# Performance work log

Hardware: AMD Instinct MI355X
Metric: run time of the kernel (lower is better)

The kernel has to match this reference:

```python
import jax, jax.numpy as jnp
import numpy as np
import math

L = 6; D = 768; NH = 12; DH = D // NH; V = 2048; CTX = 512; B = 16; T = 512
PAD_ID = 0; PAD_X = 18; PAD_Y = 32; N_ACTIONS = 9


def _layernorm(x, s, b, eps=1e-5):
    m = jnp.mean(x, axis=-1, keepdims=True)
    v = jnp.mean((x - m) ** 2, axis=-1, keepdims=True)
    return (x - m) * jax.lax.rsqrt(v + eps) * s + b


def setup_inputs() -> dict:
    key = jax.random.key(0)
    ks = jax.random.split(key, 16)
    s = 0.02
    x_emb = jax.random.normal(ks[4], (19, D), jnp.float32) * s
    x_emb = x_emb.at[PAD_X].set(0.0)  # padding_idx row is zero in torch
    y_emb = jax.random.normal(ks[5], (33, D), jnp.float32) * s
    y_emb = y_emb.at[PAD_Y].set(0.0)
    return {
        "history_cards": jax.random.randint(ks[0], (B, T), 0, V),
        "history_players": jax.random.randint(ks[1], (B, T), 0, 2),
        "deck": jax.random.randint(ks[2], (B, 8), 0, V),
        "opp_deck": jax.random.randint(ks[3], (B, 8), 0, V),
        "tok_emb": jax.random.normal(ks[6], (V, D), jnp.float32) * s,
        "player_emb": jax.random.normal(ks[7], (2, D), jnp.float32) * s,
        "pos_emb": jax.random.normal(ks[8], (CTX, D), jnp.float32) * s,
        "x_emb": x_emb,
        "y_emb": y_emb,
        "ln1_s": jnp.ones((L, D), jnp.float32),
        "ln1_b": jnp.zeros((L, D), jnp.float32),
        "qkv_w": jax.random.normal(ks[9], (L, D, 3 * D), jnp.float32) * s,
        "qkv_b": jnp.zeros((L, 3 * D), jnp.float32),
        "proj_w": jax.random.normal(ks[10], (L, D, D), jnp.float32) * s,
        "proj_b": jnp.zeros((L, D), jnp.float32),
        "ln2_s": jnp.ones((L, D), jnp.float32),
        "ln2_b": jnp.zeros((L, D), jnp.float32),
        "fc1_w": jax.random.normal(ks[11], (L, D, 4 * D), jnp.float32) * s,
        "fc1_b": jnp.zeros((L, 4 * D), jnp.float32),
        "fc2_w": jax.random.normal(ks[12], (L, 4 * D, D), jnp.float32) * s,
        "fc2_b": jnp.zeros((L, D), jnp.float32),
        "lnf_s": jnp.ones((D,), jnp.float32),
        "lnf_b": jnp.zeros((D,), jnp.float32),
        "head_w": jax.random.normal(ks[13], (D, N_ACTIONS), jnp.float32) * s,
        "head_b": jnp.zeros((N_ACTIONS,), jnp.float32),
    }


def reference(history_cards, history_players, deck, opp_deck,
              tok_emb, player_emb, pos_emb, x_emb, y_emb,
              ln1_s, ln1_b, qkv_w, qkv_b, proj_w, proj_b,
              ln2_s, ln2_b, fc1_w, fc1_b, fc2_w, fc2_b,
              lnf_s, lnf_b, head_w, head_b):
    Bc, Tc = history_cards.shape
    attn_mask = history_cards != PAD_ID                      # (B,T) True = valid
    all_pad = ~jnp.any(attn_mask, axis=1)
    attn_mask = attn_mask.at[:, 0].set(attn_mask[:, 0] | all_pad)

    # multi-embedding sum (history_x/history_y are None => padding rows = 0)
    h = (tok_emb[history_cards]
         + player_emb[jnp.clip(history_players, 0, 1)]
         + x_emb[PAD_X] + y_emb[PAD_Y]
         + jnp.mean(tok_emb[deck], axis=1, keepdims=True)
         + jnp.mean(tok_emb[opp_deck], axis=1, keepdims=True))
    x = h + pos_emb[:Tc][None]                               # (B,T,D)

    causal = jnp.tril(jnp.ones((Tc, Tc), bool))
    mask = causal[None, None, :, :] & attn_mask[:, None, None, :]  # (B,1,T,T)
    neg_inf = jnp.float32(-jnp.inf)
    scale = 1.0 / math.sqrt(DH)

    for i in range(L):
        # attention
        xn = _layernorm(x, ln1_s[i], ln1_b[i])
        qkv = xn @ qkv_w[i] + qkv_b[i]
        q, k, v = jnp.split(qkv, 3, axis=-1)
        q = q.reshape(Bc, Tc, NH, DH)
        k = k.reshape(Bc, Tc, NH, DH)
        v = v.reshape(Bc, Tc, NH, DH)
        scores = jnp.einsum('bihd,bjhd->bhij', q, k) * scale
        scores = jnp.where(mask, scores, neg_inf)
        w = jax.nn.softmax(scores, axis=-1)
        w = jnp.nan_to_num(w, nan=0.0, posinf=0.0, neginf=0.0)
        y = jnp.einsum('bhij,bjhd->bihd', w, v).reshape(Bc, Tc, D)
        x = x + (y @ proj_w[i] + proj_b[i])
        # MLP
        xn = _layernorm(x, ln2_s[i], ln2_b[i])
        hmid = jax.nn.gelu(xn @ fc1_w[i] + fc1_b[i], approximate=False)
        x = x + (hmid @ fc2_w[i] + fc2_b[i])

    x = _layernorm(x, lnf_s, lnf_b)
    last_idx = jnp.clip(jnp.sum(attn_mask.astype(jnp.int32), axis=1) - 1, 0, None)
    last_h = x[jnp.arange(Bc), last_idx]                     # (B,D)
    return last_h @ head_w + head_b                          # (B,9)
```

## Files before the change

kernel.cpp:

```cpp
#include <hip/hip_runtime.h>
#include <hip/hip_bf16.h>
#include <math.h>

typedef __hip_bfloat16 bf16;
typedef __bf16 bf16x8 __attribute__((ext_vector_type(8)));
typedef float f32x4 __attribute__((ext_vector_type(4)));

__device__ __forceinline__ float b2f(bf16 v){ return __bfloat162float(v); }
__device__ __forceinline__ bf16  f2b(float v){ return __float2bfloat16(v); }

__device__ __forceinline__ float gelu_f(float v){
    float y = v * (1.f + 0.044715f * v * v);
    return v / (1.f + __expf(-1.5957691216057308f * y));
}

__device__ __forceinline__ void gl_lds16(const bf16* g, bf16* l) {
    __builtin_amdgcn_global_load_lds((const __attribute__((address_space(1))) unsigned int*)g,
                                     (__attribute__((address_space(3))) unsigned int*)l, 16, 0, 0);
}

__device__ __forceinline__ uint2 pack4bf(const float* v){
    union { unsigned short e[4]; uint2 u; } pk;
    #pragma unroll
    for (int r = 0; r < 4; r++) pk.e[r] = __builtin_bit_cast(unsigned short, f2b(v[r]));
    return pk.u;
}

__global__ __launch_bounds__(256) void deckmean_k(const int* __restrict__ deck, const int* __restrict__ opp,
                                                  const float* __restrict__ tok, float* __restrict__ deckm)
{
    int b = blockIdx.x, w = blockIdx.y;
    const int* dk = (w ? opp : deck) + b * 8;
    int idx[8];
    #pragma unroll
    for (int j = 0; j < 8; j++) idx[j] = dk[j];
    float* out = deckm + (size_t)(w * 16 + b) * 768;
    for (int d = threadIdx.x; d < 768; d += 256) {
        float s = 0.f;
        #pragma unroll
        for (int j = 0; j < 8; j++) s += tok[(size_t)idx[j] * 768 + d];
        out[d] = s * 0.125f;
    }
}

__global__ __launch_bounds__(512) void mask_k(const int* __restrict__ cards, int* __restrict__ maskb,
                                              int* __restrict__ lastidx)
{
    int b = blockIdx.x, t = threadIdx.x;
    int m = (cards[b * 512 + t] != 0) ? 1 : 0;
    maskb[b * 512 + t] = m;
    __shared__ int red[512];
    red[t] = m; __syncthreads();
    for (int st = 256; st > 0; st >>= 1) { if (t < st) red[t] += red[t + st]; __syncthreads(); }
    if (t == 0) {
        int cnt = red[0];
        if (cnt == 0) { maskb[b * 512] = 1; cnt = 1; }
        lastidx[b] = cnt - 1;
    }
}

__global__ __launch_bounds__(256) void embed_k(const int* __restrict__ cards, const int* __restrict__ players,
                                               const float* __restrict__ tok, const float* __restrict__ pemb,
                                               const float* __restrict__ pos, const float* __restrict__ deckm,
                                               float* __restrict__ x)
{
    int t = blockIdx.x;
    int b = t >> 9, ti = t & 511;
    int cd = cards[t];
    int p = players[t]; p = p < 0 ? 0 : (p > 1 ? 1 : p);
    const float* tr  = tok  + (size_t)cd * 768;
    const float* pr  = pemb + (size_t)p  * 768;
    const float* po  = pos  + (size_t)ti * 768;
    const float* dm = deckm + (size_t)b * 768;
    const float* om = deckm + (size_t)(16 + b) * 768;
    float* xr = x + (size_t)t * 768;
    for (int d = threadIdx.x; d < 768; d += 256)
        xr[d] = tr[d] + pr[d] + po[d] + dm[d] + om[d];
}

__global__ __launch_bounds__(192) void ln_k(const float* __restrict__ x, const float* __restrict__ s,
                                            const float* __restrict__ b, bf16* __restrict__ out)
{
    int row = blockIdx.x, tid = threadIdx.x;
    float4 v = ((const float4*)(x + (size_t)row * 768))[tid];
    float sum = v.x + v.y + v.z + v.w;
    float sq  = v.x * v.x + v.y * v.y + v.z * v.z + v.w * v.w;
    #pragma unroll
    for (int off = 32; off > 0; off >>= 1) {
        sum += __shfl_xor(sum, off, 64);
        sq  += __shfl_xor(sq,  off, 64);
    }
    __shared__ float red[6];
    int wv = tid >> 6;
    if ((tid & 63) == 0) { red[wv] = sum; red[3 + wv] = sq; }
    __syncthreads();
    float S = red[0] + red[1] + red[2];
    float Q = red[3] + red[4] + red[5];
    float mean = S * (1.f / 768.f);
    float var  = Q * (1.f / 768.f) - mean * mean;
    float rstd = rsqrtf(var + 1e-5f);
    float4 sv = ((const float4*)s)[tid];
    float4 bv = ((const float4*)b)[tid];
    float o[4] = { (v.x - mean) * rstd * sv.x + bv.x, (v.y - mean) * rstd * sv.y + bv.y,
                   (v.z - mean) * rstd * sv.z + bv.z, (v.w - mean) * rstd * sv.w + bv.w };
    ((uint2*)(out + (size_t)row * 768))[tid] = pack4bf(o);
}

__global__ __launch_bounds__(256) void transpose4_k(const float* __restrict__ qw, const float* __restrict__ pw,
                                                    const float* __restrict__ f1, const float* __restrict__ f2,
                                                    bf16* __restrict__ oq, bf16* __restrict__ op,
                                                    bf16* __restrict__ o1, bf16* __restrict__ o2)
{
    int t = blockIdx.x;
    const float* in; bf16* out; int K, N, nbx;
    if (t < 432)       { in = qw; out = oq; K = 768;  N = 2304; nbx = 36; }
    else if (t < 576)  { in = pw; out = op; K = 768;  N = 768;  t -= 432;  nbx = 12; }
    else if (t < 1152) { in = f1; out = o1; K = 768;  N = 3072; t -= 576;  nbx = 48; }
    else               { in = f2; out = o2; K = 3072; N = 768;  t -= 1152; nbx = 12; }
    int n0 = (t % nbx) * 64, k0 = (t / nbx) * 64;
    int kq = threadIdx.x & 15, nq = threadIdx.x >> 4;
    float4 rr[4];
    #pragma unroll
    for (int r = 0; r < 4; r++)
        rr[r] = *(const float4*)&in[(size_t)(k0 + kq * 4 + r) * N + n0 + nq * 4];
    const float* fp = (const float*)rr;
    #pragma unroll
    for (int c = 0; c < 4; c++) {
        float v[4] = { fp[c], fp[4 + c], fp[8 + c], fp[12 + c] };
        *(uint2*)&out[(size_t)(n0 + nq * 4 + c) * K + k0 + kq * 4] = pack4bf(v);
    }
}

__global__ __launch_bounds__(256) void gemm128_k(const bf16* __restrict__ A, const bf16* __restrict__ BT,
                                                 const float* __restrict__ bias,
                                                 float* __restrict__ outF, bf16* __restrict__ outB,
                                                 int N, int K, int act, int nb)
{
    __shared__ __align__(16) bf16 Al[128 * 64];
    __shared__ __align__(16) bf16 Bl[128 * 64];
    const int tid = threadIdx.x;
    const int lane = tid & 63, wave = tid >> 6;
    const int quad = lane >> 4, l16 = lane & 15;
    const int wm = wave >> 1, wn = wave & 1;

    const int bid = blockIdx.x;
    const int xcd = bid & 7, slot = bid >> 3;
    const int m_loc = slot / nb, nbl = slot - m_loc * nb;
    const int m0 = (xcd * 8 + m_loc) * 128, n0 = nbl * 128;

    f32x4 acc[4][4] = {};
    const int srow = wave * 32;
    const int grow = srow + (lane >> 3);
    const int gcol = (lane & 7) * 8;

    for (int k0 = 0; k0 < K; k0 += 64) {
        #pragma unroll
        for (int i = 0; i < 4; i++) {
            gl_lds16(&A [(size_t)(m0 + grow + i * 8) * K + k0 + gcol], &Al[(srow + i * 8) * 64]);
            gl_lds16(&BT[(size_t)(n0 + grow + i * 8) * K + k0 + gcol], &Bl[(srow + i * 8) * 64]);
        }
        __syncthreads();
        #pragma unroll
        for (int kk = 0; kk < 64; kk += 32) {
            bf16x8 af[4], bfr[4];
            #pragma unroll
            for (int t = 0; t < 4; t++) {
                af[t]  = __builtin_bit_cast(bf16x8, *(const uint4*)(&Al[(wm * 64 + t * 16 + l16) * 64 + kk + quad * 8]));
                bfr[t] = __builtin_bit_cast(bf16x8, *(const uint4*)(&Bl[(wn * 64 + t * 16 + l16) * 64 + kk + quad * 8]));
            }
            #pragma unroll
            for (int tm = 0; tm < 4; tm++)
                #pragma unroll
                for (int tn = 0; tn < 4; tn++)
                    acc[tm][tn] = __builtin_amdgcn_mfma_f32_16x16x32_bf16(bfr[tn], af[tm], acc[tm][tn], 0, 0, 0);
        }
        __syncthreads();
    }

    float4 bv[4];
    #pragma unroll
    for (int tn = 0; tn < 4; tn++)
        bv[tn] = *(const float4*)&bias[n0 + wn * 64 + tn * 16 + quad * 4];

    #pragma unroll
    for (int tm = 0; tm < 4; tm++) {
        int m = m0 + wm * 64 + tm * 16 + l16;
        #pragma unroll
        for (int tn = 0; tn < 4; tn++) {
            int nbase = n0 + wn * 64 + tn * 16 + quad * 4;
            float v[4] = { acc[tm][tn][0] + bv[tn].x, acc[tm][tn][1] + bv[tn].y,
                           acc[tm][tn][2] + bv[tn].z, acc[tm][tn][3] + bv[tn].w };
            if (act) {
                #pragma unroll
                for (int r = 0; r < 4; r++) v[r] = gelu_f(v[r]);
            }
            size_t off = (size_t)m * N + nbase;
            if (outB) *(uint2*)&outB[off] = pack4bf(v);
            else      *(float4*)&outF[off] = make_float4(v[0], v[1], v[2], v[3]);
        }
    }
}

__global__ __launch_bounds__(256) void gemm64_k(const bf16* __restrict__ A, const bf16* __restrict__ BT,
                                                const float* __restrict__ bias,
                                                float* __restrict__ x, int N, int K, int nb)
{
    __shared__ __align__(16) bf16 Al[64 * 64];
    __shared__ __align__(16) bf16 Bl[128 * 64];
    const int tid = threadIdx.x;
    const int lane = tid & 63, wave = tid >> 6;
    const int quad = lane >> 4, l16 = lane & 15;
    const int wm = wave >> 1, wn = wave & 1;

    const int bid = blockIdx.x;
    const int xcd = bid & 7, slot = bid >> 3;
    const int m_loc = slot / nb, nbl = slot - m_loc * nb;
    const int m0 = (xcd * 16 + m_loc) * 64, n0 = nbl * 128;

    f32x4 acc[2][4] = {};
    const int srow = wave * 8 + (lane >> 3);
    const int gcol = (lane & 7) * 8;

    for (int k0 = 0; k0 < K; k0 += 64) {
        #pragma unroll
        for (int i = 0; i < 2; i++)
            gl_lds16(&A [(size_t)(m0 + srow + i * 32) * K + k0 + gcol], &Al[(wave * 8 + i * 32) * 64]);
        #pragma unroll
        for (int i = 0; i < 4; i++)
            gl_lds16(&BT[(size_t)(n0 + srow + i * 32) * K + k0 + gcol], &Bl[(wave * 8 + i * 32) * 64]);
        __syncthreads();
        #pragma unroll
        for (int kk = 0; kk < 64; kk += 32) {
            bf16x8 af[2], bfr[4];
            #pragma unroll
            for (int t = 0; t < 2; t++)
                af[t]  = __builtin_bit_cast(bf16x8, *(const uint4*)(&Al[(wm * 32 + t * 16 + l16) * 64 + kk + quad * 8]));
            #pragma unroll
            for (int t = 0; t < 4; t++)
                bfr[t] = __builtin_bit_cast(bf16x8, *(const uint4*)(&Bl[(wn * 64 + t * 16 + l16) * 64 + kk + quad * 8]));
            #pragma unroll
            for (int tm = 0; tm < 2; tm++)
                #pragma unroll
                for (int tn = 0; tn < 4; tn++)
                    acc[tm][tn] = __builtin_amdgcn_mfma_f32_16x16x32_bf16(bfr[tn], af[tm], acc[tm][tn], 0, 0, 0);
        }
        __syncthreads();
    }

    float4 bv[4];
    #pragma unroll
    for (int tn = 0; tn < 4; tn++)
        bv[tn] = *(const float4*)&bias[n0 + wn * 64 + tn * 16 + quad * 4];

    #pragma unroll
    for (int tm = 0; tm < 2; tm++) {
        int m = m0 + wm * 32 + tm * 16 + l16;
        #pragma unroll
        for (int tn = 0; tn < 4; tn++) {
            int nbase = n0 + wn * 64 + tn * 16 + quad * 4;
            float* xp = &x[(size_t)m * N + nbase];
            float4 xo = *(float4*)xp;
            xo.x += acc[tm][tn][0] + bv[tn].x;
            xo.y += acc[tm][tn][1] + bv[tn].y;
            xo.z += acc[tm][tn][2] + bv[tn].z;
            xo.w += acc[tm][tn][3] + bv[tn].w;
            *(float4*)xp = xo;
        }
    }
}

__global__ __launch_bounds__(256) void attn_k(const bf16* __restrict__ qkv, const int* __restrict__ mask,
                                              bf16* __restrict__ y)
{
    const int qt = blockIdx.x, h = blockIdx.y, b = blockIdx.z;
    const int qbase = qt * 128, tokb = b * 512;
    __shared__ __align__(16) unsigned short Kl[128][72];
    __shared__ __align__(16) unsigned short Vt[64][136];
    __shared__ __align__(16) unsigned short Ptq[4][16][136];
    __shared__ float mkf[128];

    const int tid = threadIdx.x, wave = tid >> 6, lane = tid & 63;
    const int quad = lane >> 4, l16 = lane & 15;

    bf16x8 bq[2][2];
    #pragma unroll
    for (int qc = 0; qc < 2; qc++) {
        const bf16* qp = &qkv[(size_t)(tokb + qbase + wave * 32 + qc * 16 + l16) * 2304 + h * 64];
        bq[qc][0] = __builtin_bit_cast(bf16x8, *(const uint4*)(qp + quad * 8));
        bq[qc][1] = __builtin_bit_cast(bf16x8, *(const uint4*)(qp + 32 + quad * 8));
    }

    float m_i[2] = { -INFINITY, -INFINITY }, l_i[2] = { 0.f, 0.f };
    f32x4 Oacc[2][4] = {};

    const int nst = qt + 1;
    for (int s = 0; s < nst; s++) {
        const int j0 = s * 128;
        __syncthreads();
        {
            int key = tid >> 1, c0 = (tid & 1) * 32;
            const bf16* kg = &qkv[(size_t)(tokb + j0 + key) * 2304 + 768  + h * 64 + c0];
            const bf16* vg = &qkv[(size_t)(tokb + j0 + key) * 2304 + 1536 + h * 64 + c0];
            #pragma unroll
            for (int q = 0; q < 4; q++)
                *(uint4*)&Kl[key][c0 + q * 8] = *(const uint4*)(kg + q * 8);
            union { uint4 u[4]; unsigned short e[32]; } vv;
            #pragma unroll
            for (int q = 0; q < 4; q++) vv.u[q] = *(const uint4*)(vg + q * 8);
            #pragma unroll
            for (int j = 0; j < 32; j++) Vt[c0 + j][key] = vv.e[j];
            if (tid < 128) mkf[tid] = mask[b * 512 + j0 + tid] ? 0.f : -INFINITY;
        }
        __syncthreads();

        #pragma unroll
        for (int qc = 0; qc < 2; qc++) {
            const int qi = qbase + wave * 32 + qc * 16 + l16;

            f32x4 sc[8] = {};
            #pragma unroll
            for (int kcc = 0; kcc < 8; kcc++) {
                bf16x8 af0 = __builtin_bit_cast(bf16x8, *(const uint4*)&Kl[kcc * 16 + l16][quad * 8]);
                bf16x8 af1 = __builtin_bit_cast(bf16x8, *(const uint4*)&Kl[kcc * 16 + l16][32 + quad * 8]);
                sc[kcc] = __builtin_amdgcn_mfma_f32_16x16x32_bf16(af0, bq[qc][0], sc[kcc], 0, 0, 0);
                sc[kcc] = __builtin_amdgcn_mfma_f32_16x16x32_bf16(af1, bq[qc][1], sc[kcc], 0, 0, 0);
            }

            float pv[8][4];
            float mx = -INFINITY;
            #pragma unroll
            for (int kcc = 0; kcc < 8; kcc++) {
                float4 mk4 = *(const float4*)&mkf[kcc * 16 + quad * 4];
                float mkr[4] = { mk4.x, mk4.y, mk4.z, mk4.w };
                #pragma unroll
                for (int r = 0; r < 4; r++) {
                    int krel = kcc * 16 + quad * 4 + r;
                    float sval = (j0 + krel <= qi) ? (sc[kcc][r] * 0.125f + mkr[r]) : -INFINITY;
                    pv[kcc][r] = sval;
                    mx = fmaxf(mx, sval);
                }
            }
            mx = fmaxf(mx, __shfl_xor(mx, 16, 64));
            mx = fmaxf(mx, __shfl_xor(mx, 32, 64));
            float mn = fmaxf(m_i[qc], mx);
            float alpha = (mn == -INFINITY) ? 1.f : __expf(m_i[qc] - mn);
            float lsum = 0.f;
            #pragma unroll
            for (int kcc = 0; kcc < 8; kcc++)
                #pragma unroll
                for (int r = 0; r < 4; r++) {
                    float pp = (pv[kcc][r] == -INFINITY) ? 0.f : __expf(pv[kcc][r] - mn);
                    pv[kcc][r] = pp; lsum += pp;
                }
            lsum += __shfl_xor(lsum, 16, 64);
            lsum += __shfl_xor(lsum, 32, 64);
            m_i[qc] = mn; l_i[qc] = alpha * l_i[qc] + lsum;

            #pragma unroll
            for (int kcc = 0; kcc < 8; kcc++)
                *(uint2*)&Ptq[wave][l16][kcc * 16 + quad * 4] = pack4bf(pv[kcc]);
            #pragma unroll
            for (int mc = 0; mc < 4; mc++)
                #pragma unroll
                for (int r = 0; r < 4; r++) Oacc[qc][mc][r] *= alpha;

            __syncthreads();

            #pragma unroll
            for (int kcc = 0; kcc < 4; kcc++) {
                bf16x8 pb = __builtin_bit_cast(bf16x8, *(const uint4*)&Ptq[wave][l16][kcc * 32 + quad * 8]);
                #pragma unroll
                for (int mc = 0; mc < 4; mc++) {
                    bf16x8 vf = __builtin_bit_cast(bf16x8, *(const uint4*)&Vt[mc * 16 + l16][kcc * 32 + quad * 8]);
                    Oacc[qc][mc] = __builtin_amdgcn_mfma_f32_16x16x32_bf16(vf, pb, Oacc[qc][mc], 0, 0, 0);
                }
            }
        }
    }

    #pragma unroll
    for (int qc = 0; qc < 2; qc++) {
        float inv = (l_i[qc] > 0.f) ? 1.f / l_i[qc] : 0.f;
        const int tok = tokb + qbase + wave * 32 + qc * 16 + l16;
        #pragma unroll
        for (int mc = 0; mc < 4; mc++) {
            float v[4] = { Oacc[qc][mc][0] * inv, Oacc[qc][mc][1] * inv,
                           Oacc[qc][mc][2] * inv, Oacc[qc][mc][3] * inv };
            *(uint2*)&y[(size_t)tok * 768 + h * 64 + mc * 16 + quad * 4] = pack4bf(v);
        }
    }
}

__global__ __launch_bounds__(256) void head_k(const float* __restrict__ x, const int* __restrict__ lastidx,
                                              const float* __restrict__ ls, const float* __restrict__ lb,
                                              const float* __restrict__ hw, const float* __restrict__ hb,
                                              float* __restrict__ out)
{
    int b = blockIdx.x, tid = threadIdx.x;
    const float* xr = x + ((size_t)(b * 512 + lastidx[b])) * 768;
    float v0 = xr[tid], v1 = xr[tid + 256], v2 = xr[tid + 512];
    __shared__ float rs[256], rq[256];
    rs[tid] = v0 + v1 + v2; rq[tid] = v0 * v0 + v1 * v1 + v2 * v2;
    __syncthreads();
    for (int st = 128; st > 0; st >>= 1) {
        if (tid < st) { rs[tid] += rs[tid + st]; rq[tid] += rq[tid + st]; }
        __syncthreads();
    }
    float mean = rs[0] * (1.f / 768.f);
    float var  = rq[0] * (1.f / 768.f) - mean * mean;
    float rstd = rsqrtf(var + 1e-5f);
    float part[9];
    #pragma unroll
    for (int a = 0; a < 9; a++) part[a] = 0.f;
    float vv[3] = { v0, v1, v2 };
    #pragma unroll
    for (int e = 0; e < 3; e++) {
        int d = tid + e * 256;
        float xnv = (vv[e] - mean) * rstd * ls[d] + lb[d];
        #pragma unroll
        for (int a = 0; a < 9; a++) part[a] += xnv * hw[d * 9 + a];
    }
    __shared__ float r9[9][256];
    #pragma unroll
    for (int a = 0; a < 9; a++) r9[a][tid] = part[a];
    __syncthreads();
    for (int st = 128; st > 0; st >>= 1) {
        if (tid < st) {
            for (int a = 0; a < 9; a++) r9[a][tid] += r9[a][tid + st];
        }
        __syncthreads();
    }
    if (tid < 9) out[b * 9 + tid] = r9[tid][0] + hb[tid];
}

extern "C" void kernel_launch(void* const* d_in, const int* in_sizes, int n_in,
                              void* d_out, int out_size, void* d_ws, size_t ws_size,
                              hipStream_t stream) {
    const int*   cards   = (const int*)  d_in[0];
    const int*   players = (const int*)  d_in[1];
    const int*   deck    = (const int*)  d_in[2];
    const int*   oppd    = (const int*)  d_in[3];
    const float* tok     = (const float*)d_in[4];
    const float* pemb    = (const float*)d_in[5];
    const float* pos     = (const float*)d_in[6];
    const float* ln1s  = (const float*)d_in[9];
    const float* ln1b  = (const float*)d_in[10];
    const float* qkvw  = (const float*)d_in[11];
    const float* qkvb  = (const float*)d_in[12];
    const float* projw = (const float*)d_in[13];
    const float* projb = (const float*)d_in[14];
    const float* ln2s  = (const float*)d_in[15];
    const float* ln2b  = (const float*)d_in[16];
    const float* fc1w  = (const float*)d_in[17];
    const float* fc1b  = (const float*)d_in[18];
    const float* fc2w  = (const float*)d_in[19];
    const float* fc2b  = (const float*)d_in[20];
    const float* lnfs  = (const float*)d_in[21];
    const float* lnfb  = (const float*)d_in[22];
    const float* hw    = (const float*)d_in[23];
    const float* hb    = (const float*)d_in[24];
    float* out = (float*)d_out;

    char* p = (char*)d_ws;
    auto alloc = [&](size_t bytes) { char* q = p; p += (bytes + 255) & ~((size_t)255); return q; };
    float* x     = (float*)alloc(8192ull * 768 * 4);
    bf16*  xn    = (bf16*) alloc(8192ull * 768 * 2);
    bf16*  big   = (bf16*) alloc(8192ull * 3072 * 2);
    bf16*  wt    = (bf16*) alloc(7077888ull * 2);
    float* deckm = (float*)alloc(2ull * 16 * 768 * 4);
    int*   maskb = (int*)  alloc(8192ull * 4);
    int*   lasti = (int*)  alloc(64);

    bf16* wq = wt;
    bf16* wp = wq + 2304ull * 768;
    bf16* w1 = wp + 768ull * 768;
    bf16* w2 = w1 + 3072ull * 768;

    deckmean_k<<<dim3(16, 2), 256, 0, stream>>>(deck, oppd, tok, deckm);
    mask_k<<<16, 512, 0, stream>>>(cards, maskb, lasti);
    embed_k<<<8192, 256, 0, stream>>>(cards, players, tok, pemb, pos, deckm, x);

    for (int i = 0; i < 6; i++) {
        transpose4_k<<<1728, 256, 0, stream>>>(
            qkvw + (size_t)i * 768 * 2304, projw + (size_t)i * 768 * 768,
            fc1w + (size_t)i * 768 * 3072, fc2w + (size_t)i * 3072 * 768,
            wq, wp, w1, w2);

        ln_k<<<8192, 192, 0, stream>>>(x, ln1s + i * 768, ln1b + i * 768, xn);
        gemm128_k<<<64 * 18, 256, 0, stream>>>(xn, wq, qkvb + i * 2304, nullptr, big, 2304, 768, 0, 18);
        attn_k<<<dim3(4, 12, 16), 256, 0, stream>>>(big, maskb, xn);
        gemm64_k<<<128 * 6, 256, 0, stream>>>(xn, wp, projb + i * 768, x, 768, 768, 6);
        ln_k<<<8192, 192, 0, stream>>>(x, ln2s + i * 768, ln2b + i * 768, xn);
        gemm128_k<<<64 * 24, 256, 0, stream>>>(xn, w1, fc1b + i * 3072, nullptr, big, 3072, 768, 1, 24);
        gemm64_k<<<128 * 6, 256, 0, stream>>>(big, w2, fc2b + i * 768, x, 768, 3072, 6);
    }

    head_k<<<16, 256, 0, stream>>>(x, lasti, lnfs, lnfb, hw, hb, out);
}
```

Measured before the change: 2.050 ms.

## Replace 128x128 GEMM with double-buffered 256x256 swizzled-LDS MFMA kernel

Swaps the QKV and FC1 GEMM kernel for a 512-thread, 256x256-tile kernel. It double-buffers A and B tiles in LDS, prefetches the next K-tile while issuing MFMAs, and XOR-swizzles the LDS layout to avoid bank conflicts. It adds explicit barriers, waitcnt control and setprio around MFMA bursts, and remaps workgroups across XCDs. The aim is more data reuse per loaded tile and hiding global-load latency. The cost is 128KB of LDS per block, which limits occupancy, and a small grid (288 and 384 blocks) that may leave an unbalanced tail on the CUs.

```diff
diff --git a/kernel.cpp b/kernel.cpp
--- a/kernel.cpp
+++ b/kernel.cpp
@@ -24,6 +24,12 @@
     #pragma unroll
     for (int r = 0; r < 4; r++) pk.e[r] = __builtin_bit_cast(unsigned short, f2b(v[r]));
     return pk.u;
+}
+
+__device__ __forceinline__ void phase_bar() {
+    __builtin_amdgcn_sched_barrier(0);
+    __builtin_amdgcn_s_barrier();
+    __builtin_amdgcn_sched_barrier(0);
 }
 
 __global__ __launch_bounds__(256) void deckmean_k(const int* __restrict__ deck, const int* __restrict__ opp,
@@ -131,74 +137,122 @@
     }
 }
 
-__global__ __launch_bounds__(256) void gemm128_k(const bf16* __restrict__ A, const bf16* __restrict__ BT,
-                                                 const float* __restrict__ bias,
-                                                 float* __restrict__ outF, bf16* __restrict__ outB,
-                                                 int N, int K, int act, int nb)
-{
-    __shared__ __align__(16) bf16 Al[128 * 64];
-    __shared__ __align__(16) bf16 Bl[128 * 64];
-    const int tid = threadIdx.x;
-    const int lane = tid & 63, wave = tid >> 6;
+__global__ __launch_bounds__(512, 2) void gemm256_k(const bf16* __restrict__ A, const bf16* __restrict__ BT,
+                                                    const float* __restrict__ bias, bf16* __restrict__ out,
+                                                    int N, int K, int act, int nbn)
+{
+    __shared__ __align__(16) bf16 Asb[2][256 * 64];
+    __shared__ __align__(16) bf16 Bsb[2][256 * 64];
+
+    const int tid  = threadIdx.x;
+    const int lane = tid & 63, wid = tid >> 6;
     const int quad = lane >> 4, l16 = lane & 15;
-    const int wm = wave >> 1, wn = wave & 1;
-
-    const int bid = blockIdx.x;
-    const int xcd = bid & 7, slot = bid >> 3;
-    const int m_loc = slot / nb, nbl = slot - m_loc * nb;
-    const int m0 = (xcd * 8 + m_loc) * 128, n0 = nbl * 128;
-
-    f32x4 acc[4][4] = {};
-    const int srow = wave * 32;
-    const int grow = srow + (lane >> 3);
-    const int gcol = (lane & 7) * 8;
-
-    for (int k0 = 0; k0 < K; k0 += 64) {
-        #pragma unroll
-        for (int i = 0; i < 4; i++) {
-            gl_lds16(&A [(size_t)(m0 + grow + i * 8) * K + k0 + gcol], &Al[(srow + i * 8) * 64]);
-            gl_lds16(&BT[(size_t)(n0 + grow + i * 8) * K + k0 + gcol], &Bl[(srow + i * 8) * 64]);
-        }
-        __syncthreads();
-        #pragma unroll
-        for (int kk = 0; kk < 64; kk += 32) {
-            bf16x8 af[4], bfr[4];
-            #pragma unroll
-            for (int t = 0; t < 4; t++) {
-                af[t]  = __builtin_bit_cast(bf16x8, *(const uint4*)(&Al[(wm * 64 + t * 16 + l16) * 64 + kk + quad * 8]));
-                bfr[t] = __builtin_bit_cast(bf16x8, *(const uint4*)(&Bl[(wn * 64 + t * 16 + l16) * 64 + kk + quad * 8]));
-            }
-            #pragma unroll
-            for (int tm = 0; tm < 4; tm++)
-                #pragma unroll
-                for (int tn = 0; tn < 4; tn++)
-                    acc[tm][tn] = __builtin_amdgcn_mfma_f32_16x16x32_bf16(bfr[tn], af[tm], acc[tm][tn], 0, 0, 0);
-        }
-        __syncthreads();
+    const int wr = wid >> 2, wc = wid & 3;
+    const int xr  = l16 & 7;
+    const int cg0 = quad ^ xr;
+    const int cg1 = cg0 ^ 4;
+
+    const int nwg  = gridDim.x;
+    const int wgid = ((int)blockIdx.x & 7) * (nwg >> 3) + ((int)blockIdx.x >> 3);
+    const int mt = wgid / nbn, nt = wgid - mt * nbn;
+    const int m0 = mt * 256, n0 = nt * 256;
+
+    const int srow = wid * 8 + (lane >> 3);
+    const int scg  = (lane & 7) ^ (lane >> 3);
+    const bf16* sa[4]; const bf16* sb[4];
+    #pragma unroll
+    for (int s = 0; s < 4; s++) {
+        sa[s] = A  + (size_t)(m0 + s * 64 + srow) * K + scg * 8;
+        sb[s] = BT + (size_t)(n0 + s * 64 + srow) * K + scg * 8;
+    }
+
+#define STG_A(s, b) gl_lds16(sa[s], &Asb[b][((s) * 64 + wid * 8) * 64])
+#define STG_B(s, b) gl_lds16(sb[s], &Bsb[b][((s) * 64 + wid * 8) * 64])
+#define LD_B(cg) { _Pragma("unroll") for (int ni = 0; ni < 4; ni++) \
+    bfv[ni] = __builtin_bit_cast(bf16x8, *(const uint4*)&Bc[(wc * 64 + ni * 16 + l16) * 64 + (cg) * 8]); }
+#define LD_A(rb, cg) { _Pragma("unroll") for (int mi = 0; mi < 4; mi++) \
+    afv[mi] = __builtin_bit_cast(bf16x8, *(const uint4*)&Ac[(wr * 128 + (rb) + mi * 16 + l16) * 64 + (cg) * 8]); }
+#define MFMA16(MB) { _Pragma("unroll") for (int mi = 0; mi < 4; mi++) \
+    _Pragma("unroll") for (int ni = 0; ni < 4; ni++) \
+        acc[(MB) + mi][ni] = __builtin_amdgcn_mfma_f32_16x16x32_bf16(bfv[ni], afv[mi], acc[(MB) + mi][ni], 0, 0, 0); }
+
+    STG_A(0, 0); STG_A(2, 0);
+    STG_B(0, 0); STG_B(1, 0); STG_B(2, 0); STG_B(3, 0);
+    STG_A(1, 0); STG_A(3, 0);
+    #pragma unroll
+    for (int s = 0; s < 4; s++) { sa[s] += 64; sb[s] += 64; }
+
+    f32x4 acc[8][4] = {};
+
+    asm volatile("s_waitcnt vmcnt(2)" ::: "memory");
+    phase_bar();
+
+    const int NKT = K >> 6;
+    for (int kt = 0; kt < NKT; kt++) {
+        const bf16* Ac = Asb[kt & 1];
+        const bf16* Bc = Bsb[kt & 1];
+        const int nxt = (kt & 1) ^ 1;
+        const bool pf = (kt + 1 < NKT);
+        bf16x8 bfv[4], afv[4];
+
+        LD_B(cg0); LD_A(0, cg0);
+        if (pf) {
+            STG_A(0, nxt); STG_A(2, nxt);
+            STG_B(0, nxt); STG_B(1, nxt); STG_B(2, nxt); STG_B(3, nxt);
+            asm volatile("s_waitcnt vmcnt(6)" ::: "memory");
+        } else {
+            asm volatile("s_waitcnt vmcnt(0)" ::: "memory");
+        }
+        phase_bar();
+        __builtin_amdgcn_s_setprio(1); MFMA16(0); __builtin_amdgcn_s_setprio(0);
+        phase_bar();
+
+        LD_A(64, cg0);
+        if (pf) { STG_A(1, nxt); STG_A(3, nxt); }
+        phase_bar();
+        __builtin_amdgcn_s_setprio(1); MFMA16(4); __builtin_amdgcn_s_setprio(0);
+        phase_bar();
+
+        LD_B(cg1); LD_A(0, cg1);
+        phase_bar();
+        __builtin_amdgcn_s_setprio(1); MFMA16(0); __builtin_amdgcn_s_setprio(0);
+        phase_bar();
+
+        LD_A(64, cg1);
+        phase_bar();
+        __builtin_amdgcn_s_setprio(1); MFMA16(4); __builtin_amdgcn_s_setprio(0);
+        asm volatile("s_waitcnt vmcnt(2)" ::: "memory");
+        phase_bar();
+
+        #pragma unroll
+        for (int s = 0; s < 4; s++) { sa[s] += 64; sb[s] += 64; }
     }
 
     float4 bv[4];
     #pragma unroll
-    for (int tn = 0; tn < 4; tn++)
-        bv[tn] = *(const float4*)&bias[n0 + wn * 64 + tn * 16 + quad * 4];
-
-    #pragma unroll
-    for (int tm = 0; tm < 4; tm++) {
-        int m = m0 + wm * 64 + tm * 16 + l16;
-        #pragma unroll
-        for (int tn = 0; tn < 4; tn++) {
-            int nbase = n0 + wn * 64 + tn * 16 + quad * 4;
-            float v[4] = { acc[tm][tn][0] + bv[tn].x, acc[tm][tn][1] + bv[tn].y,
-                           acc[tm][tn][2] + bv[tn].z, acc[tm][tn][3] + bv[tn].w };
+    for (int ni = 0; ni < 4; ni++)
+        bv[ni] = *(const float4*)&bias[n0 + wc * 64 + ni * 16 + quad * 4];
+
+    #pragma unroll
+    for (int mi = 0; mi < 8; mi++) {
+        const int m = m0 + wr * 128 + mi * 16 + l16;
+        #pragma unroll
+        for (int ni = 0; ni < 4; ni++) {
+            const int nb2 = n0 + wc * 64 + ni * 16 + quad * 4;
+            float v[4] = { acc[mi][ni][0] + bv[ni].x, acc[mi][ni][1] + bv[ni].y,
+                           acc[mi][ni][2] + bv[ni].z, acc[mi][ni][3] + bv[ni].w };
             if (act) {
                 #pragma unroll
                 for (int r = 0; r < 4; r++) v[r] = gelu_f(v[r]);
             }
-            size_t off = (size_t)m * N + nbase;
-            if (outB) *(uint2*)&outB[off] = pack4bf(v);
-            else      *(float4*)&outF[off] = make_float4(v[0], v[1], v[2], v[3]);
-        }
-    }
+            *(uint2*)&out[(size_t)m * N + nb2] = pack4bf(v);
+        }
+    }
+#undef STG_A
+#undef STG_B
+#undef LD_B
+#undef LD_A
+#undef MFMA16
 }
 
 __global__ __launch_bounds__(256) void gemm64_k(const bf16* __restrict__ A, const bf16* __restrict__ BT,
@@ -487,11 +541,11 @@
             wq, wp, w1, w2);
 
         ln_k<<<8192, 192, 0, stream>>>(x, ln1s + i * 768, ln1b + i * 768, xn);
-        gemm128_k<<<64 * 18, 256, 0, stream>>>(xn, wq, qkvb + i * 2304, nullptr, big, 2304, 768, 0, 18);
+        gemm256_k<<<288, 512, 0, stream>>>(xn, wq, qkvb + i * 2304, big, 2304, 768, 0, 9);
         attn_k<<<dim3(4, 12, 16), 256, 0, stream>>>(big, maskb, xn);
         gemm64_k<<<128 * 6, 256, 0, stream>>>(xn, wp, projb + i * 768, x, 768, 768, 6);
         ln_k<<<8192, 192, 0, stream>>>(x, ln2s + i * 768, ln2b + i * 768, xn);
-        gemm128_k<<<64 * 24, 256, 0, stream>>>(xn, w1, fc1b + i * 3072, nullptr, big, 3072, 768, 1, 24);
+        gemm256_k<<<384, 512, 0, stream>>>(xn, w1, fc1b + i * 3072, big, 3072, 768, 1, 12);
         gemm64_k<<<128 * 6, 256, 0, stream>>>(big, w2, fc2b + i * 768, x, 768, 3072, 6);
     }
 
```

Result: faster. 1.997 ms (-2.6%).
